# Performance work log

Measured on AMD Instinct MI355X. Metric: run time of the kernel, lower is better.

Reference implementation:

```python
import jax, jax.numpy as jnp
import numpy as np

N_NODES = 50000
N_EDGES = 800000
FEAT = 64
HID = 128
N_TYPES = 4
N_REL = 3
N_LAYERS = 2
LN_EPS = 1e-5


def setup_inputs() -> dict:
    key = jax.random.key(0)
    ks = jax.random.split(key, 20)
    inp = {
        "z": jax.random.randint(ks[0], (N_NODES,), 0, 100, dtype=jnp.int32),
        "node_type": jax.random.randint(ks[1], (N_NODES,), 0, N_TYPES, dtype=jnp.int32),
        "edge_index": jax.random.randint(ks[2], (2, N_EDGES), 0, N_NODES, dtype=jnp.int32),
        "edge_type": jax.random.randint(ks[3], (N_EDGES,), 0, N_REL, dtype=jnp.int32),
        # learned parameters
        "z_embed": jax.random.normal(ks[4], (100, FEAT), jnp.float32),
        "enc_w1": jax.random.normal(ks[5], (N_TYPES, FEAT, HID), jnp.float32) * 0.05,
        "enc_b1": jnp.zeros((N_TYPES, HID), jnp.float32),
        "enc_w2": jax.random.normal(ks[6], (N_TYPES, HID, HID), jnp.float32) * 0.05,
        "enc_b2": jnp.zeros((N_TYPES, HID), jnp.float32),
        "lin_w": jax.random.normal(ks[7], (N_LAYERS, HID, HID), jnp.float32) * 0.05,
        "lin_b": jnp.zeros((N_LAYERS, HID), jnp.float32),
        "rel_w": jax.random.normal(ks[8], (N_LAYERS, N_REL, HID, HID), jnp.float32) * 0.05,
        "ln_g": jnp.ones((N_LAYERS, HID), jnp.float32),
        "ln_b": jnp.zeros((N_LAYERS, HID), jnp.float32),
        "reg_w": jax.random.normal(ks[9], (HID, 1), jnp.float32) * 0.05,
        "reg_b": jnp.zeros((1,), jnp.float32),
    }
    return inp


def _layer_norm(x, g, b):
    mu = jnp.mean(x, axis=-1, keepdims=True)
    var = jnp.mean((x - mu) ** 2, axis=-1, keepdims=True)
    return (x - mu) * jax.lax.rsqrt(var + LN_EPS) * g + b


def reference(z, node_type, edge_index, edge_type, z_embed, enc_w1, enc_b1,
              enc_w2, enc_b2, lin_w, lin_b, rel_w, ln_g, ln_b, reg_w, reg_b):
    n = z.shape[0]
    # FeatureBuilder (site_ads=None path): atomic-number embedding lookup
    raw = z_embed[z]  # [N, FEAT]
    # TypeSpecificEncoder: run all 4 type MLPs, select per node by node_type
    h = jax.nn.relu(jnp.einsum('nd,tdh->nth', raw, enc_w1) + enc_b1)  # [N,T,H]
    enc_all = jnp.einsum('nth,tho->nto', h, enc_w2) + enc_b2           # [N,T,H]
    x = jnp.take_along_axis(enc_all, node_type[:, None, None].astype(jnp.int32), axis=1)[:, 0, :]

    src, dst = edge_index[0], edge_index[1]
    deg = jax.ops.segment_sum(jnp.ones((edge_type.shape[0],), x.dtype), dst, num_segments=n)
    deg = jnp.clip(deg, 1.0, None)[:, None]  # [N,1]

    for l in range(N_LAYERS):
        out = jnp.zeros_like(x)
        x_src = x[src]  # [E, H] gathered source features
        for r in range(N_REL):
            mask = (edge_type == r).astype(x.dtype)[:, None]
            msg = (x_src * mask) @ rel_w[l, r]  # [E, H]
            out = out + jax.ops.segment_sum(msg, dst, num_segments=n)
        out = out / deg
        x = _layer_norm(x @ lin_w[l] + lin_b[l] + out, ln_g[l], ln_b[l])

    pooled = jnp.mean(x, axis=0)  # mean pooling, mask = all ones
    return pooled @ reg_w + reg_b  # [1]
```

## Files before the change

kernel.cpp:

```cpp
#include <hip/hip_runtime.h>

#define N_NODES 50000
#define N_EDGES 800000
#define FEAT 64
#define HID 128
#define N_TYPES 4
#define N_REL 3
#define N_LAYERS 2
#define LN_EPS 1e-5f
#define NROWS 50016
#define NG32 1563
#define CAP 64
#define NBKT 196
#define CAP1 4608
#define EPB 4096
#define BINCAP 56
#define NCOMBO 400
#define WT_STRIDE 136

typedef __attribute__((ext_vector_type(8))) short bf16x8;
typedef __attribute__((ext_vector_type(16))) float f32x16;
typedef __attribute__((ext_vector_type(2))) float f32x2;

static __device__ inline unsigned short f2bf(float f) {
    unsigned int u = __float_as_uint(f);
    return (unsigned short)((u + 0x7fffu + ((u >> 16) & 1u)) >> 16);
}
static __device__ inline unsigned int packbf2(float lo, float hi) {
    return (unsigned int)f2bf(lo) | ((unsigned int)f2bf(hi) << 16);
}

static __device__ inline void acc8_fp8(float* a, uint2 w) {
    f32x2 d0 = __builtin_amdgcn_cvt_pk_f32_fp8((int)w.x, false);
    f32x2 d1 = __builtin_amdgcn_cvt_pk_f32_fp8((int)w.x, true);
    f32x2 d2 = __builtin_amdgcn_cvt_pk_f32_fp8((int)w.y, false);
    f32x2 d3 = __builtin_amdgcn_cvt_pk_f32_fp8((int)w.y, true);
    a[0] += d0[0]; a[1] += d0[1]; a[2] += d1[0]; a[3] += d1[1];
    a[4] += d2[0]; a[5] += d2[1]; a[6] += d3[0]; a[7] += d3[1];
}

__global__ __launch_bounds__(256) void bin1_kernel(const int* __restrict__ src,
                                                   const int* __restrict__ dst,
                                                   const int* __restrict__ et,
                                                   const int* __restrict__ z,
                                                   const int* __restrict__ nt,
                                                   unsigned short* __restrict__ combo,
                                                   int* __restrict__ bcnt,
                                                   int* __restrict__ bucket) {
    int ci = blockIdx.x * 256 + threadIdx.x;
    if (ci < N_NODES) combo[ci] = (unsigned short)(z[ci] * 4 + nt[ci]);

    __shared__ int lbin[NBKT * BINCAP];
    __shared__ int lcnt[NBKT];
    __shared__ int lbase[NBKT];
    for (int i = threadIdx.x; i < NBKT; i += 256) lcnt[i] = 0;
    __syncthreads();
    int base = blockIdx.x * EPB;
#pragma unroll
    for (int i = 0; i < EPB / 256; ++i) {
        int e = base + i * 256 + threadIdx.x;
        if (e < N_EDGES) {
            int d = dst[e];
            int b = d >> 8;
            int v = src[e] | (et[e] << 16) | ((d & 255) << 18);
            int pos = atomicAdd(&lcnt[b], 1);
            if (pos < BINCAP) lbin[b * BINCAP + pos] = v;
        }
    }
    __syncthreads();
    if (threadIdx.x < NBKT) {
        int c = min(lcnt[threadIdx.x], BINCAP);
        lcnt[threadIdx.x] = c;
        lbase[threadIdx.x] = atomicAdd(&bcnt[threadIdx.x], c);
    }
    __syncthreads();
    int wv = threadIdx.x >> 6, ln = threadIdx.x & 63;
    for (int b = wv; b < NBKT; b += 4) {
        int c = lcnt[b];
        if (ln < c) {
            int gp = lbase[b] + ln;
            if (gp < CAP1) bucket[b * CAP1 + gp] = lbin[b * BINCAP + ln];
        }
    }
}

__global__ __launch_bounds__(256) void build2_kernel(const int* __restrict__ bcnt,
                                                     const int* __restrict__ bucket,
                                                     const unsigned short* __restrict__ combo,
                                                     int* __restrict__ cnt3,
                                                     int* __restrict__ payload) {
    __shared__ int lcnt[256 * 3];
    for (int i = threadIdx.x; i < 768; i += 256) lcnt[i] = 0;
    __syncthreads();
    int b = blockIdx.x;
    int n0 = b << 8;
    int cb = min(bcnt[b], CAP1);
    const int* bk = bucket + b * CAP1;
    for (int i = threadIdx.x; i < cb; i += 256) {
        int v = bk[i];
        atomicAdd(&lcnt[((v >> 18) & 255) * 3 + ((v >> 16) & 3)], 1);
    }
    __syncthreads();
    int t = threadIdx.x;
    int c0 = min(lcnt[t * 3 + 0], CAP);
    int c1 = min(lcnt[t * 3 + 1], CAP - c0);
    int c2 = min(lcnt[t * 3 + 2], CAP - c0 - c1);
    __syncthreads();
    lcnt[t * 3 + 0] = 0;
    lcnt[t * 3 + 1] = c0;
    lcnt[t * 3 + 2] = c0 + c1;
    int node = n0 + t;
    if (node < N_NODES) cnt3[node] = c0 | (c1 << 8) | (c2 << 16);
    __syncthreads();
    for (int i = threadIdx.x; i < cb; i += 256) {
        int v = bk[i];
        int dl = (v >> 18) & 255;
        int r = (v >> 16) & 3;
        int sc = v & 0xffff;
        int pos = atomicAdd(&lcnt[dl * 3 + r], 1);
        if (pos < CAP)
            payload[((n0 + dl) << 6) + pos] = sc | ((int)combo[sc] << 18);
    }
}

__global__ __launch_bounds__(128) void table_kernel(const float* __restrict__ z_embed,
                                                    const float* __restrict__ w1,
                                                    const float* __restrict__ b1,
                                                    const float* __restrict__ w2,
                                                    const float* __restrict__ b2,
                                                    const float* __restrict__ rel_w,
                                                    const float* __restrict__ lin_w,
                                                    const float* __restrict__ lin_b,
                                                    unsigned int* __restrict__ ytab,
                                                    float* __restrict__ lintab,
                                                    unsigned short* __restrict__ wbuf,
                                                    float* __restrict__ pooled) {
    if (blockIdx.x >= NCOMBO) {
        int pb = blockIdx.x - NCOMBO;
        if (pb == 0) pooled[threadIdx.x] = 0.0f;
        int idx = pb * 128 + threadIdx.x;
        int k = idx & 127;
        int col = (idx >> 7) & 127;
        int mat = idx >> 14;
        float w = (mat < 3) ? rel_w[(((size_t)(3 + mat)) * HID + k) * HID + col]
                            : lin_w[((size_t)(HID + k)) * HID + col];
        wbuf[(size_t)mat * HID * WT_STRIDE + col * WT_STRIDE + k] = f2bf(w);
        return;
    }
    int c = blockIdx.x;
    int zi = c >> 2;
    int t = c & 3;
    int j = threadIdx.x;
    __shared__ float h[HID];
    __shared__ float xrow[HID];
    __shared__ float tmp[HID];
    float acc = b1[t * HID + j];
#pragma unroll 8
    for (int k = 0; k < FEAT; ++k)
        acc = fmaf(z_embed[zi * FEAT + k], w1[((size_t)t * FEAT + k) * HID + j], acc);
    h[j] = fmaxf(acc, 0.0f);
    __syncthreads();
    float acc2 = b2[t * HID + j];
#pragma unroll 8
    for (int k = 0; k < HID; ++k)
        acc2 = fmaf(h[k], w2[(size_t)t * HID * HID + k * HID + j], acc2);
    xrow[j] = acc2;
    __syncthreads();
#pragma unroll 1
    for (int r = 0; r < N_REL; ++r) {
        float a = 0.f;
        const float* W = rel_w + (size_t)r * HID * HID;
#pragma unroll 8
        for (int k = 0; k < HID; ++k) a = fmaf(xrow[k], W[k * HID + j], a);
        tmp[j] = a;
        __syncthreads();
        if (j < 32) {
            int w0 = __builtin_amdgcn_cvt_pk_fp8_f32(tmp[4 * j], tmp[4 * j + 1], 0, false);
            w0 = __builtin_amdgcn_cvt_pk_fp8_f32(tmp[4 * j + 2], tmp[4 * j + 3], w0, true);
            ytab[(r * NCOMBO + c) * 32 + j] = (unsigned)w0;
        }
        __syncthreads();
    }
    float a = lin_b[j];
#pragma unroll 8
    for (int k = 0; k < HID; ++k) a = fmaf(xrow[k], lin_w[k * HID + j], a);
    lintab[c * HID + j] = a;
}

__global__ __launch_bounds__(256) void gather_ln1_kernel(
    const int* __restrict__ cnt3, const int* __restrict__ payload,
    const uint2* __restrict__ ytab8, const float* __restrict__ lintab,
    const unsigned short* __restrict__ combo, const float* __restrict__ lng,
    const float* __restrict__ lnb, uint4* __restrict__ xb4,
    uint2* __restrict__ xf8) {
    int tid = blockIdx.x * 256 + threadIdx.x;
    int node = tid >> 4;
    int l16 = tid & 15;
    int c3 = cnt3[node];
    int c0 = c3 & 255, c1 = (c3 >> 8) & 255, c2 = (c3 >> 16) & 255;
    int tot = c0 + c1 + c2;
    float inv = 1.0f / (float)max(tot, 1);
    const int* pl = payload + (node << 6);
    float a[8] = {};
    int e = 0;
#pragma unroll 1
    for (int r = 0; r < 3; ++r) {
        int e1 = (r == 0) ? c0 : (r == 1) ? c0 + c1 : tot;
        int base = (r * NCOMBO) << 4;
        for (; e + 2 <= e1; e += 2) {
            int pA = pl[e], pB = pl[e + 1];
            uint2 vA = ytab8[base + ((pA >> 18) << 4) + l16];
            uint2 vB = ytab8[base + ((pB >> 18) << 4) + l16];
            acc8_fp8(a, vA);
            acc8_fp8(a, vB);
        }
        if (e < e1) {
            int p = pl[e]; ++e;
            acc8_fp8(a, ytab8[base + ((p >> 18) << 4) + l16]);
        }
    }
    const float* lrow = lintab + (int)combo[node] * HID + l16 * 8;
    float v[8], s = 0.f, q = 0.f;
#pragma unroll
    for (int j = 0; j < 8; ++j) {
        v[j] = fmaf(a[j], inv, lrow[j]);
        s += v[j];
        q += v[j] * v[j];
    }
#pragma unroll
    for (int mk = 1; mk < 16; mk <<= 1) {
        s += __shfl_xor(s, mk);
        q += __shfl_xor(q, mk);
    }
    float mu = s * (1.0f / HID);
    float rstd = rsqrtf(q * (1.0f / HID) - mu * mu + LN_EPS);
    const float* g8 = lng + l16 * 8;
    const float* b8 = lnb + l16 * 8;
    float o[8];
#pragma unroll
    for (int j = 0; j < 8; ++j) o[j] = (v[j] - mu) * rstd * g8[j] + b8[j];
    uint4 w;
    w.x = packbf2(o[0], o[1]);
    w.y = packbf2(o[2], o[3]);
    w.z = packbf2(o[4], o[5]);
    w.w = packbf2(o[6], o[7]);
    xb4[(node << 4) + l16] = w;
    int lo = 0, hi = 0;
    lo = __builtin_amdgcn_cvt_pk_fp8_f32(o[0], o[1], lo, false);
    lo = __builtin_amdgcn_cvt_pk_fp8_f32(o[2], o[3], lo, true);
    hi = __builtin_amdgcn_cvt_pk_fp8_f32(o[4], o[5], hi, false);
    hi = __builtin_amdgcn_cvt_pk_fp8_f32(o[6], o[7], hi, true);
    xf8[(node << 4) + l16] = make_uint2((unsigned)lo, (unsigned)hi);
}

__global__ __launch_bounds__(256) void gather3_kernel(const int* __restrict__ cnt3,
                                                      const int* __restrict__ payload,
                                                      const uint2* __restrict__ xf8,
                                                      uint4* __restrict__ s0,
                                                      uint4* __restrict__ s1,
                                                      uint4* __restrict__ s2) {
    int tid = blockIdx.x * 256 + threadIdx.x;
    int node = tid >> 4;
    int l16 = tid & 15;
    int c3 = cnt3[node];
    int c0 = c3 & 255, c1 = (c3 >> 8) & 255, c2 = (c3 >> 16) & 255;
    int tot = c0 + c1 + c2;
    float inv = 1.0f / (float)max(tot, 1);
    const int* pl = payload + (node << 6);
    int o = node * 16 + l16;
    int e = 0;
#pragma unroll 1
    for (int r = 0; r < 3; ++r) {
        int e1 = (r == 0) ? c0 : (r == 1) ? c0 + c1 : tot;
        float a[8] = {};
        for (; e + 2 <= e1; e += 2) {
            int pA = pl[e], pB = pl[e + 1];
            uint2 vA = xf8[((pA & 0xffff) << 4) + l16];
            uint2 vB = xf8[((pB & 0xffff) << 4) + l16];
            acc8_fp8(a, vA);
            acc8_fp8(a, vB);
        }
        if (e < e1) {
            int p = pl[e]; ++e;
            acc8_fp8(a, xf8[((p & 0xffff) << 4) + l16]);
        }
        uint4 w;
        w.x = packbf2(a[0] * inv, a[1] * inv);
        w.y = packbf2(a[2] * inv, a[3] * inv);
        w.z = packbf2(a[4] * inv, a[5] * inv);
        w.w = packbf2(a[6] * inv, a[7] * inv);
        if (r == 0) s0[o] = w;
        else if (r == 1) s1[o] = w;
        else s2[o] = w;
    }
}

__global__ __launch_bounds__(512) void fused_layer_kernel(
    const unsigned short* __restrict__ s0, const unsigned short* __restrict__ s1,
    const unsigned short* __restrict__ s2, const unsigned short* __restrict__ xb,
    const uint4* __restrict__ wbuf, const float* __restrict__ lb,
    const float* __restrict__ lng, const float* __restrict__ lnb,
    float* __restrict__ pooled) {
    __shared__ __align__(16) unsigned short Wt[4 * HID * WT_STRIDE];
    __shared__ float csh[3 * HID];
    __shared__ float pooled_sh[HID];

    if (threadIdx.x < HID) {
        pooled_sh[threadIdx.x] = 0.0f;
        csh[threadIdx.x] = lb[threadIdx.x];
        csh[HID + threadIdx.x] = lng[threadIdx.x];
        csh[2 * HID + threadIdx.x] = lnb[threadIdx.x];
    }
    uint4* wt4 = (uint4*)Wt;
#pragma unroll
    for (int i = 0; i < 17; ++i)
        wt4[i * 512 + threadIdx.x] = wbuf[i * 512 + threadIdx.x];
    __syncthreads();

    int wave = threadIdx.x >> 6;
    int lane = threadIdx.x & 63;
    int n32 = lane & 31;
    int hf = lane >> 5;

    float pacc[4] = {0.f, 0.f, 0.f, 0.f};

    for (int g = wave * gridDim.x + blockIdx.x; g < NG32; g += gridDim.x * 8) {
        int node0 = g * 32;
        f32x16 acc[4];
#pragma unroll
        for (int ct = 0; ct < 4; ++ct)
#pragma unroll
            for (int i = 0; i < 16; ++i) acc[ct][i] = 0.0f;

#pragma unroll 1
        for (int mat = 0; mat < 4; ++mat) {
            const unsigned short* asrc = (mat == 0) ? s0 : (mat == 1) ? s1
                                       : (mat == 2) ? s2 : xb;
            const unsigned short* arow = asrc + (size_t)(node0 + n32) * HID + hf * 8;
            const unsigned short* wm = Wt + mat * (HID * WT_STRIDE) + n32 * WT_STRIDE + hf * 8;
#pragma unroll 2
            for (int t = 0; t < 8; ++t) {
                bf16x8 a = *(const bf16x8*)(arow + t * 16);
#pragma unroll
                for (int ct = 0; ct < 4; ++ct) {
                    bf16x8 b = *(const bf16x8*)(wm + ct * 32 * WT_STRIDE + t * 16);
                    acc[ct] = __builtin_amdgcn_mfma_f32_32x32x16_bf16(a, b, acc[ct], 0, 0, 0);
                }
            }
        }
#pragma unroll
        for (int reg = 0; reg < 16; ++reg) {
            int row = node0 + (reg & 3) + 8 * (reg >> 2) + 4 * hf;
            float v[4];
            float s = 0.f, q = 0.f;
#pragma unroll
            for (int ct = 0; ct < 4; ++ct) {
                v[ct] = acc[ct][reg] + csh[ct * 32 + n32];
                s += v[ct];
                q += v[ct] * v[ct];
            }
#pragma unroll
            for (int mk = 1; mk < 32; mk <<= 1) {
                s += __shfl_xor(s, mk);
                q += __shfl_xor(q, mk);
            }
            float mu = s * (1.0f / HID);
            float rstd = rsqrtf(q * (1.0f / HID) - mu * mu + LN_EPS);
            if (row < N_NODES) {
#pragma unroll
                for (int ct = 0; ct < 4; ++ct) {
                    int col = ct * 32 + n32;
                    pacc[ct] += (v[ct] - mu) * rstd * csh[HID + col] + csh[2 * HID + col];
                }
            }
        }
    }

#pragma unroll
    for (int ct = 0; ct < 4; ++ct) {
        float t = pacc[ct] + __shfl_xor(pacc[ct], 32);
        if (hf == 0) atomicAdd(&pooled_sh[ct * 32 + n32], t);
    }
    __syncthreads();
    if (threadIdx.x < HID) atomicAdd(&pooled[threadIdx.x], pooled_sh[threadIdx.x]);
}

__global__ void final_kernel(const float* __restrict__ pooled, const float* __restrict__ reg_w,
                             const float* __restrict__ reg_b, float* __restrict__ out) {
    int lane = threadIdx.x;
    float s = pooled[lane] * reg_w[lane] + pooled[64 + lane] * reg_w[64 + lane];
#pragma unroll
    for (int o = 32; o; o >>= 1) s += __shfl_down(s, o);
    if (lane == 0) out[0] = s * (1.0f / N_NODES) + reg_b[0];
}

extern "C" void kernel_launch(void* const* d_in, const int* in_sizes, int n_in,
                              void* d_out, int out_size, void* d_ws, size_t ws_size,
                              hipStream_t stream) {
    const int* z = (const int*)d_in[0];
    const int* nt = (const int*)d_in[1];
    const int* ei = (const int*)d_in[2];
    const int* et = (const int*)d_in[3];
    const float* z_embed = (const float*)d_in[4];
    const float* enc_w1 = (const float*)d_in[5];
    const float* enc_b1 = (const float*)d_in[6];
    const float* enc_w2 = (const float*)d_in[7];
    const float* enc_b2 = (const float*)d_in[8];
    const float* lin_w = (const float*)d_in[9];
    const float* lin_b = (const float*)d_in[10];
    const float* rel_w = (const float*)d_in[11];
    const float* ln_g = (const float*)d_in[12];
    const float* ln_b = (const float*)d_in[13];
    const float* reg_w = (const float*)d_in[14];
    const float* reg_b = (const float*)d_in[15];
    float* out = (float*)d_out;

    const size_t NHb = (size_t)NROWS * HID;
    char* p = (char*)d_ws;
    unsigned short* xb = (unsigned short*)p;    p += NHb * 2;
    unsigned short* s0 = (unsigned short*)p;    p += NHb * 2;
    unsigned short* s1 = (unsigned short*)p;    p += NHb * 2;
    unsigned short* s2 = (unsigned short*)p;    p += NHb * 2;
    uint2* xf8 = (uint2*)p;                     p += NHb;
    unsigned short* wbuf = (unsigned short*)p;  p += (size_t)4 * HID * WT_STRIDE * 2;
    unsigned int* ytab = (unsigned int*)p;      p += (size_t)N_REL * NCOMBO * HID;
    float* lintab = (float*)p;                  p += NCOMBO * HID * 4;
    unsigned short* combo = (unsigned short*)p; p += N_NODES * 2;
    float* pooled = (float*)p;                  p += HID * 4;
    int* cnt3 = (int*)p;                        p += N_NODES * 4;
    int* bcnt = (int*)p;                        p += NBKT * 4;
    int* bucket = (int*)p;                      p += (size_t)NBKT * CAP1 * 4;
    int* payload = (int*)p;                     p += (size_t)N_NODES * CAP * 4;

    const int* src = ei;
    const int* dst = ei + N_EDGES;

    hipMemsetAsync(bcnt, 0, NBKT * sizeof(int), stream);
    bin1_kernel<<<NBKT, 256, 0, stream>>>(src, dst, et, z, nt, combo, bcnt, bucket);
    build2_kernel<<<NBKT, 256, 0, stream>>>(bcnt, bucket, combo, cnt3, payload);

    table_kernel<<<NCOMBO + 512, 128, 0, stream>>>(z_embed, enc_w1, enc_b1, enc_w2, enc_b2,
                                                   rel_w, lin_w, lin_b, ytab, lintab,
                                                   wbuf, pooled);

    gather_ln1_kernel<<<3125, 256, 0, stream>>>(cnt3, payload, (const uint2*)ytab, lintab,
                                                combo, ln_g, ln_b, (uint4*)xb, xf8);
    gather3_kernel<<<3125, 256, 0, stream>>>(cnt3, payload, xf8,
                                             (uint4*)s0, (uint4*)s1, (uint4*)s2);
    fused_layer_kernel<<<256, 512, 0, stream>>>(
        s0, s1, s2, xb, (const uint4*)wbuf, lin_b + HID, ln_g + HID, ln_b + HID, pooled);

    final_kernel<<<1, 64, 0, stream>>>(pooled, reg_w, reg_b, out);
}
```

Before: 233.5 us.

## Merge binning and table kernels, fold final reduction, unroll gathers by four

The edge-binning kernel and the per-combo encoder/table kernel become one launch with block ranges for each role, run at 256 threads with the table blocks masked to 128 active lanes. The final regression dot product moves into the last block of the fused layer kernel through a done-counter and threadfence, which removes a separate launch. The fp8 gather loops in both gather kernels are unrolled from two to four edges per iteration to keep more loads in flight. Together these cut launch count and serialisation, at the cost of a larger shared-memory footprint for the merged kernel, idle threads in the table blocks, and a global atomic counter.

```diff
diff --git a/kernel.cpp b/kernel.cpp
--- a/kernel.cpp
+++ b/kernel.cpp
@@ -39,48 +39,115 @@
     a[4] += d2[0]; a[5] += d2[1]; a[6] += d3[0]; a[7] += d3[1];
 }
 
-__global__ __launch_bounds__(256) void bin1_kernel(const int* __restrict__ src,
-                                                   const int* __restrict__ dst,
-                                                   const int* __restrict__ et,
-                                                   const int* __restrict__ z,
-                                                   const int* __restrict__ nt,
-                                                   unsigned short* __restrict__ combo,
-                                                   int* __restrict__ bcnt,
-                                                   int* __restrict__ bucket) {
-    int ci = blockIdx.x * 256 + threadIdx.x;
-    if (ci < N_NODES) combo[ci] = (unsigned short)(z[ci] * 4 + nt[ci]);
-
+__global__ __launch_bounds__(256) void build_tables_kernel(
+    const int* __restrict__ src, const int* __restrict__ dst,
+    const int* __restrict__ et, const int* __restrict__ z,
+    const int* __restrict__ nt,
+    const float* __restrict__ z_embed, const float* __restrict__ w1,
+    const float* __restrict__ b1, const float* __restrict__ w2,
+    const float* __restrict__ b2, const float* __restrict__ rel_w,
+    const float* __restrict__ lin_w, const float* __restrict__ lin_b,
+    unsigned short* __restrict__ combo, int* __restrict__ bcnt,
+    int* __restrict__ bucket, unsigned int* __restrict__ ytab,
+    float* __restrict__ lintab, unsigned short* __restrict__ wbuf,
+    float* __restrict__ pooled) {
     __shared__ int lbin[NBKT * BINCAP];
     __shared__ int lcnt[NBKT];
     __shared__ int lbase[NBKT];
-    for (int i = threadIdx.x; i < NBKT; i += 256) lcnt[i] = 0;
-    __syncthreads();
-    int base = blockIdx.x * EPB;
-#pragma unroll
-    for (int i = 0; i < EPB / 256; ++i) {
-        int e = base + i * 256 + threadIdx.x;
-        if (e < N_EDGES) {
-            int d = dst[e];
-            int b = d >> 8;
-            int v = src[e] | (et[e] << 16) | ((d & 255) << 18);
-            int pos = atomicAdd(&lcnt[b], 1);
-            if (pos < BINCAP) lbin[b * BINCAP + pos] = v;
-        }
-    }
-    __syncthreads();
-    if (threadIdx.x < NBKT) {
-        int c = min(lcnt[threadIdx.x], BINCAP);
-        lcnt[threadIdx.x] = c;
-        lbase[threadIdx.x] = atomicAdd(&bcnt[threadIdx.x], c);
-    }
-    __syncthreads();
-    int wv = threadIdx.x >> 6, ln = threadIdx.x & 63;
-    for (int b = wv; b < NBKT; b += 4) {
-        int c = lcnt[b];
-        if (ln < c) {
-            int gp = lbase[b] + ln;
-            if (gp < CAP1) bucket[b * CAP1 + gp] = lbin[b * BINCAP + ln];
-        }
+    __shared__ float h[HID];
+    __shared__ float xrow[HID];
+    __shared__ float tmp[HID];
+
+    int b = blockIdx.x;
+    if (b < NBKT) {
+        int ci = b * 256 + threadIdx.x;
+        if (ci < N_NODES) combo[ci] = (unsigned short)(z[ci] * 4 + nt[ci]);
+        for (int i = threadIdx.x; i < NBKT; i += 256) lcnt[i] = 0;
+        __syncthreads();
+        int base = b * EPB;
+#pragma unroll
+        for (int i = 0; i < EPB / 256; ++i) {
+            int e = base + i * 256 + threadIdx.x;
+            if (e < N_EDGES) {
+                int d = dst[e];
+                int bk = d >> 8;
+                int v = src[e] | (et[e] << 16) | ((d & 255) << 18);
+                int pos = atomicAdd(&lcnt[bk], 1);
+                if (pos < BINCAP) lbin[bk * BINCAP + pos] = v;
+            }
+        }
+        __syncthreads();
+        if (threadIdx.x < NBKT) {
+            int c = min(lcnt[threadIdx.x], BINCAP);
+            lcnt[threadIdx.x] = c;
+            lbase[threadIdx.x] = atomicAdd(&bcnt[threadIdx.x], c);
+        }
+        __syncthreads();
+        int wv = threadIdx.x >> 6, ln = threadIdx.x & 63;
+        for (int bb = wv; bb < NBKT; bb += 4) {
+            int c = lcnt[bb];
+            if (ln < c) {
+                int gp = lbase[bb] + ln;
+                if (gp < CAP1) bucket[bb * CAP1 + gp] = lbin[bb * BINCAP + ln];
+            }
+        }
+        return;
+    }
+    if (b >= NBKT + NCOMBO) {
+        int pb = b - (NBKT + NCOMBO);
+        if (pb == 0 && threadIdx.x < HID) pooled[threadIdx.x] = 0.0f;
+        int idx = pb * 256 + threadIdx.x;
+        int k = idx & 127;
+        int col = (idx >> 7) & 127;
+        int mat = idx >> 14;
+        float w = (mat < 3) ? rel_w[(((size_t)(3 + mat)) * HID + k) * HID + col]
+                            : lin_w[((size_t)(HID + k)) * HID + col];
+        wbuf[(size_t)mat * HID * WT_STRIDE + col * WT_STRIDE + k] = f2bf(w);
+        return;
+    }
+    int c = b - NBKT;
+    int zi = c >> 2;
+    int t = c & 3;
+    int j = threadIdx.x;
+    bool act = j < HID;
+    if (act) {
+        float acc = b1[t * HID + j];
+#pragma unroll 8
+        for (int k = 0; k < FEAT; ++k)
+            acc = fmaf(z_embed[zi * FEAT + k], w1[((size_t)t * FEAT + k) * HID + j], acc);
+        h[j] = fmaxf(acc, 0.0f);
+    }
+    __syncthreads();
+    if (act) {
+        float acc2 = b2[t * HID + j];
+#pragma unroll 8
+        for (int k = 0; k < HID; ++k)
+            acc2 = fmaf(h[k], w2[(size_t)t * HID * HID + k * HID + j], acc2);
+        xrow[j] = acc2;
+    }
+    __syncthreads();
+#pragma unroll 1
+    for (int r = 0; r < N_REL; ++r) {
+        if (act) {
+            float a = 0.f;
+            const float* W = rel_w + (size_t)r * HID * HID;
+#pragma unroll 8
+            for (int k = 0; k < HID; ++k) a = fmaf(xrow[k], W[k * HID + j], a);
+            tmp[j] = a;
+        }
+        __syncthreads();
+        if (j < 32) {
+            int w0 = __builtin_amdgcn_cvt_pk_fp8_f32(tmp[4 * j], tmp[4 * j + 1], 0, false);
+            w0 = __builtin_amdgcn_cvt_pk_fp8_f32(tmp[4 * j + 2], tmp[4 * j + 3], w0, true);
+            ytab[(r * NCOMBO + c) * 32 + j] = (unsigned)w0;
+        }
+        __syncthreads();
+    }
+    if (act) {
+        float a = lin_b[j];
+#pragma unroll 8
+        for (int k = 0; k < HID; ++k) a = fmaf(xrow[k], lin_w[k * HID + j], a);
+        lintab[c * HID + j] = a;
     }
 }
 
@@ -121,70 +188,6 @@
         if (pos < CAP)
             payload[((n0 + dl) << 6) + pos] = sc | ((int)combo[sc] << 18);
     }
-}
-
-__global__ __launch_bounds__(128) void table_kernel(const float* __restrict__ z_embed,
-                                                    const float* __restrict__ w1,
-                                                    const float* __restrict__ b1,
-                                                    const float* __restrict__ w2,
-                                                    const float* __restrict__ b2,
-                                                    const float* __restrict__ rel_w,
-                                                    const float* __restrict__ lin_w,
-                                                    const float* __restrict__ lin_b,
-                                                    unsigned int* __restrict__ ytab,
-                                                    float* __restrict__ lintab,
-                                                    unsigned short* __restrict__ wbuf,
-                                                    float* __restrict__ pooled) {
-    if (blockIdx.x >= NCOMBO) {
-        int pb = blockIdx.x - NCOMBO;
-        if (pb == 0) pooled[threadIdx.x] = 0.0f;
-        int idx = pb * 128 + threadIdx.x;
-        int k = idx & 127;
-        int col = (idx >> 7) & 127;
-        int mat = idx >> 14;
-        float w = (mat < 3) ? rel_w[(((size_t)(3 + mat)) * HID + k) * HID + col]
-                            : lin_w[((size_t)(HID + k)) * HID + col];
-        wbuf[(size_t)mat * HID * WT_STRIDE + col * WT_STRIDE + k] = f2bf(w);
-        return;
-    }
-    int c = blockIdx.x;
-    int zi = c >> 2;
-    int t = c & 3;
-    int j = threadIdx.x;
-    __shared__ float h[HID];
-    __shared__ float xrow[HID];
-    __shared__ float tmp[HID];
-    float acc = b1[t * HID + j];
-#pragma unroll 8
-    for (int k = 0; k < FEAT; ++k)
-        acc = fmaf(z_embed[zi * FEAT + k], w1[((size_t)t * FEAT + k) * HID + j], acc);
-    h[j] = fmaxf(acc, 0.0f);
-    __syncthreads();
-    float acc2 = b2[t * HID + j];
-#pragma unroll 8
-    for (int k = 0; k < HID; ++k)
-        acc2 = fmaf(h[k], w2[(size_t)t * HID * HID + k * HID + j], acc2);
-    xrow[j] = acc2;
-    __syncthreads();
-#pragma unroll 1
-    for (int r = 0; r < N_REL; ++r) {
-        float a = 0.f;
-        const float* W = rel_w + (size_t)r * HID * HID;
-#pragma unroll 8
-        for (int k = 0; k < HID; ++k) a = fmaf(xrow[k], W[k * HID + j], a);
-        tmp[j] = a;
-        __syncthreads();
-        if (j < 32) {
-            int w0 = __builtin_amdgcn_cvt_pk_fp8_f32(tmp[4 * j], tmp[4 * j + 1], 0, false);
-            w0 = __builtin_amdgcn_cvt_pk_fp8_f32(tmp[4 * j + 2], tmp[4 * j + 3], w0, true);
-            ytab[(r * NCOMBO + c) * 32 + j] = (unsigned)w0;
-        }
-        __syncthreads();
-    }
-    float a = lin_b[j];
-#pragma unroll 8
-    for (int k = 0; k < HID; ++k) a = fmaf(xrow[k], lin_w[k * HID + j], a);
-    lintab[c * HID + j] = a;
 }
 
 __global__ __launch_bounds__(256) void gather_ln1_kernel(
@@ -207,12 +210,24 @@
     for (int r = 0; r < 3; ++r) {
         int e1 = (r == 0) ? c0 : (r == 1) ? c0 + c1 : tot;
         int base = (r * NCOMBO) << 4;
-        for (; e + 2 <= e1; e += 2) {
+        for (; e + 4 <= e1; e += 4) {
+            int pA = pl[e], pB = pl[e + 1], pC = pl[e + 2], pD = pl[e + 3];
+            uint2 vA = ytab8[base + ((pA >> 18) << 4) + l16];
+            uint2 vB = ytab8[base + ((pB >> 18) << 4) + l16];
+            uint2 vC = ytab8[base + ((pC >> 18) << 4) + l16];
+            uint2 vD = ytab8[base + ((pD >> 18) << 4) + l16];
+            acc8_fp8(a, vA);
+            acc8_fp8(a, vB);
+            acc8_fp8(a, vC);
+            acc8_fp8(a, vD);
+        }
+        if (e + 2 <= e1) {
             int pA = pl[e], pB = pl[e + 1];
             uint2 vA = ytab8[base + ((pA >> 18) << 4) + l16];
             uint2 vB = ytab8[base + ((pB >> 18) << 4) + l16];
             acc8_fp8(a, vA);
             acc8_fp8(a, vB);
+            e += 2;
         }
         if (e < e1) {
             int p = pl[e]; ++e;
@@ -273,12 +288,24 @@
     for (int r = 0; r < 3; ++r) {
         int e1 = (r == 0) ? c0 : (r == 1) ? c0 + c1 : tot;
         float a[8] = {};
-        for (; e + 2 <= e1; e += 2) {
+        for (; e + 4 <= e1; e += 4) {
+            int pA = pl[e], pB = pl[e + 1], pC = pl[e + 2], pD = pl[e + 3];
+            uint2 vA = xf8[((pA & 0xffff) << 4) + l16];
+            uint2 vB = xf8[((pB & 0xffff) << 4) + l16];
+            uint2 vC = xf8[((pC & 0xffff) << 4) + l16];
+            uint2 vD = xf8[((pD & 0xffff) << 4) + l16];
+            acc8_fp8(a, vA);
+            acc8_fp8(a, vB);
+            acc8_fp8(a, vC);
+            acc8_fp8(a, vD);
+        }
+        if (e + 2 <= e1) {
             int pA = pl[e], pB = pl[e + 1];
             uint2 vA = xf8[((pA & 0xffff) << 4) + l16];
             uint2 vB = xf8[((pB & 0xffff) << 4) + l16];
             acc8_fp8(a, vA);
             acc8_fp8(a, vB);
+            e += 2;
         }
         if (e < e1) {
             int p = pl[e]; ++e;
@@ -300,10 +327,13 @@
     const unsigned short* __restrict__ s2, const unsigned short* __restrict__ xb,
     const uint4* __restrict__ wbuf, const float* __restrict__ lb,
     const float* __restrict__ lng, const float* __restrict__ lnb,
-    float* __restrict__ pooled) {
+    float* __restrict__ pooled, const float* __restrict__ reg_w,
+    const float* __restrict__ reg_b, float* __restrict__ out,
+    int* __restrict__ done) {
     __shared__ __align__(16) unsigned short Wt[4 * HID * WT_STRIDE];
     __shared__ float csh[3 * HID];
     __shared__ float pooled_sh[HID];
+    __shared__ int lastFlag;
 
     if (threadIdx.x < HID) {
         pooled_sh[threadIdx.x] = 0.0f;
@@ -383,15 +413,20 @@
     }
     __syncthreads();
     if (threadIdx.x < HID) atomicAdd(&pooled[threadIdx.x], pooled_sh[threadIdx.x]);
-}
-
-__global__ void final_kernel(const float* __restrict__ pooled, const float* __restrict__ reg_w,
-                             const float* __restrict__ reg_b, float* __restrict__ out) {
-    int lane = threadIdx.x;
-    float s = pooled[lane] * reg_w[lane] + pooled[64 + lane] * reg_w[64 + lane];
-#pragma unroll
-    for (int o = 32; o; o >>= 1) s += __shfl_down(s, o);
-    if (lane == 0) out[0] = s * (1.0f / N_NODES) + reg_b[0];
+
+    __threadfence();
+    __syncthreads();
+    if (threadIdx.x == 0)
+        lastFlag = (atomicAdd(done, 1) == (int)gridDim.x - 1);
+    __syncthreads();
+    if (lastFlag && threadIdx.x < 64) {
+        int l = threadIdx.x;
+        float s = atomicAdd(&pooled[l], 0.0f) * reg_w[l] +
+                  atomicAdd(&pooled[64 + l], 0.0f) * reg_w[64 + l];
+#pragma unroll
+        for (int o = 32; o; o >>= 1) s += __shfl_down(s, o);
+        if (l == 0) out[0] = s * (1.0f / N_NODES) + reg_b[0];
+    }
 }
 
 extern "C" void kernel_launch(void* const* d_in, const int* in_sizes, int n_in,
@@ -429,26 +464,26 @@
     float* pooled = (float*)p;                  p += HID * 4;
     int* cnt3 = (int*)p;                        p += N_NODES * 4;
     int* bcnt = (int*)p;                        p += NBKT * 4;
+    int* done = (int*)p;                        p += 4;
     int* bucket = (int*)p;                      p += (size_t)NBKT * CAP1 * 4;
     int* payload = (int*)p;                     p += (size_t)N_NODES * CAP * 4;
 
     const int* src = ei;
     const int* dst = ei + N_EDGES;
 
-    hipMemsetAsync(bcnt, 0, NBKT * sizeof(int), stream);
-    bin1_kernel<<<NBKT, 256, 0, stream>>>(src, dst, et, z, nt, combo, bcnt, bucket);
+    hipMemsetAsync(bcnt, 0, (NBKT + 1) * sizeof(int), stream);
+
+    build_tables_kernel<<<NBKT + NCOMBO + 256, 256, 0, stream>>>(
+        src, dst, et, z, nt, z_embed, enc_w1, enc_b1, enc_w2, enc_b2,
+        rel_w, lin_w, lin_b, combo, bcnt, bucket, ytab, lintab, wbuf, pooled);
+
     build2_kernel<<<NBKT, 256, 0, stream>>>(bcnt, bucket, combo, cnt3, payload);
-
-    table_kernel<<<NCOMBO + 512, 128, 0, stream>>>(z_embed, enc_w1, enc_b1, enc_w2, enc_b2,
-                                                   rel_w, lin_w, lin_b, ytab, lintab,
-                                                   wbuf, pooled);
 
     gather_ln1_kernel<<<3125, 256, 0, stream>>>(cnt3, payload, (const uint2*)ytab, lintab,
                                                 combo, ln_g, ln_b, (uint4*)xb, xf8);
     gather3_kernel<<<3125, 256, 0, stream>>>(cnt3, payload, xf8,
                                              (uint4*)s0, (uint4*)s1, (uint4*)s2);
     fused_layer_kernel<<<256, 512, 0, stream>>>(
-        s0, s1, s2, xb, (const uint4*)wbuf, lin_b + HID, ln_g + HID, ln_b + HID, pooled);
-
-    final_kernel<<<1, 64, 0, stream>>>(pooled, reg_w, reg_b, out);
-}
+        s0, s1, s2, xb, (const uint4*)wbuf, lin_b + HID, ln_g + HID, ln_b + HID,
+        pooled, reg_w, reg_b, out, done);
+}
```

Measured after the change: 233.6 us. About the same (+0.0%).
